# Performance work log

Measured on AMD Instinct MI355X. Metric: run time of the kernel, lower is better.

## Reference

```python
import jax, jax.numpy as jnp
import numpy as np

B, L, K = 4, 4096, 48
BIG = 1e9  # masked-out distance sentinel


def setup_inputs() -> dict:
    key = jax.random.key(0)
    k1, k2 = jax.random.split(key)
    # Backbone coords (B, L, 4, 3): N, CA, C, O. Scaled to Angstrom-ish magnitudes.
    X = jax.random.normal(k1, (B, L, 4, 3), dtype=jnp.float32) * 10.0
    mask = (jax.random.uniform(k2, (B, L)) > 0.1).astype(jnp.float32)
    return {"X": X, "mask": mask, "k_neighbors": K}


def reference(X, mask, k_neighbors):
    """GPU-friendly equivalent of precompute_knn_cpu:
    brute-force masked pairwise euclidean distances + top-k, with
    self-fill for invalid residues and the degenerate n_valid<=k batch case.
    Returns (D_neighbors (B,L,k) float, E_idx (B,L,k) int32).
    """
    Xca = X[:, :, 1, :]                       # (B, L, 3) CA atoms
    m = mask > 0                              # (B, L) bool valid
    # ||a-b||^2 = ||a||^2 + ||b||^2 - 2 a.b  (avoids (B,L,L,3) intermediate)
    x2 = jnp.sum(Xca * Xca, axis=-1)          # (B, L)
    D2 = x2[:, :, None] + x2[:, None, :] - 2.0 * jnp.einsum('bld,bmd->blm', Xca, Xca)
    D = jnp.sqrt(jnp.maximum(D2, 0.0))        # (B, L, L)
    # mask invalid key columns so they are never selected
    Dm = jnp.where(m[:, None, :], D, BIG)
    _, idx = jax.lax.top_k(-Dm, k_neighbors)  # k smallest distances, (B, L, k)
    self_idx = jnp.broadcast_to(jnp.arange(L, dtype=idx.dtype)[None, :, None],
                                (B, L, k_neighbors))
    n_valid = jnp.sum(m, axis=1)              # (B,)
    # degenerate batch: n_valid <= k -> every row filled with its own index
    degen = (n_valid <= k_neighbors)[:, None, None]
    # invalid rows -> self index; valid rows -> knn indices (already in original index space)
    E_idx = jnp.where(degen | (~m[:, :, None]), self_idx, idx)
    D_neighbors = jnp.take_along_axis(D, E_idx, axis=2)  # (B, L, k)
    return D_neighbors, E_idx
```

## Files before the change

### kernel.cpp

```cpp
#include <hip/hip_runtime.h>

typedef unsigned long long u64;

#define L_DIM 4096
#define B_DIM 4
#define KNN 48
#define CAP 512
#define INVALID_X2 1.0e30f
#define VALID_TH 1.0e29f
#define SLACK 8u
#define NT 256
#define NW 4
#define CPT 16
#define ROWS 2

__global__ __launch_bounds__(256) void prep_kernel(const float* __restrict__ X,
                                                   const float* __restrict__ mask,
                                                   float4* __restrict__ c4,
                                                   int* __restrict__ nvalid) {
#pragma clang fp contract(off)
    int i = blockIdx.x * 256 + threadIdx.x;
    const float4* X4 = (const float4*)X;
    float4 a = X4[3 * i];
    float4 bb = X4[3 * i + 1];
    float x = a.w, y = bb.x, z = bb.y;
    float x2 = __builtin_fmaf(z, z, __builtin_fmaf(y, y, x * x));
    float m = mask[i];
    c4[i] = make_float4(x, y, z, (m > 0.0f) ? x2 : INVALID_X2);
    unsigned long long bal = __ballot(m > 0.0f);
    if ((threadIdx.x & 63) == 0)
        atomicAdd(&nvalid[i >> 12], (int)__popcll(bal));
}

__device__ __forceinline__ unsigned wave_sort64(unsigned sv, int lane) {
#pragma unroll
    for (int k = 2; k <= 64; k <<= 1) {
#pragma unroll
        for (int j = k >> 1; j > 0; j >>= 1) {
            unsigned o = __shfl_xor(sv, j);
            unsigned mn = min(sv, o), mx = max(sv, o);
            bool asc = ((lane & k) == 0);
            bool low = ((lane & j) == 0);
            sv = (asc == low) ? mn : mx;
        }
    }
    return sv;
}

__global__ __launch_bounds__(NT) void knn_kernel(const float4* __restrict__ c4,
                                                 const int* __restrict__ nvalid,
                                                 float* __restrict__ dn,
                                                 float* __restrict__ ei) {
    __shared__ unsigned gmin[ROWS][64];
    __shared__ u64 surv[ROWS][CAP];
    __shared__ int cnt[ROWS];
    __shared__ unsigned Tsh[ROWS];

    const int row0 = blockIdx.x * ROWS;
    const int b = row0 >> 12;
    const int i0 = row0 & (L_DIM - 1);
    const int t = threadIdx.x;
    const int w = t >> 6, lane = t & 63;

    if (nvalid[b] <= KNN) {
        if (w < ROWS && lane < KNN) {
            dn[(size_t)(row0 + w) * KNN + lane] = 0.0f;
            ei[(size_t)(row0 + w) * KNN + lane] = (float)(i0 + w);
        }
        return;
    }

    const float4* cb = c4 + (size_t)b * L_DIM;
    const float4 q0 = cb[i0];
    const float4 q1 = cb[i0 + 1];
    const bool v0 = (q0.w < VALID_TH), v1 = (q1.w < VALID_TH);

    unsigned d20[CPT], d21[CPT];
    unsigned rmin0 = 0xFFFFFFFFu, rmin1 = 0xFFFFFFFFu;
    {
#pragma clang fp contract(off)
#pragma unroll
        for (int c = 0; c < CPT; ++c) {
            int j = c * NT + t;
            float4 pj = cb[j];
            float dota = __builtin_fmaf(pj.z, q0.z,
                         __builtin_fmaf(pj.y, q0.y, pj.x * q0.x));
            float dotb = __builtin_fmaf(pj.z, q1.z,
                         __builtin_fmaf(pj.y, q1.y, pj.x * q1.x));
            float d2a = fmaxf(__builtin_fmaf(-2.0f, dota, q0.w + pj.w), 0.0f);
            float d2b = fmaxf(__builtin_fmaf(-2.0f, dotb, q1.w + pj.w), 0.0f);
            d20[c] = __float_as_uint(d2a);
            d21[c] = __float_as_uint(d2b);
            rmin0 = min(rmin0, d20[c]);
            rmin1 = min(rmin1, d21[c]);
        }
    }

    {
        unsigned g0 = min(rmin0, __shfl_xor(rmin0, 1));
        g0 = min(g0, __shfl_xor(g0, 2));
        unsigned g1 = min(rmin1, __shfl_xor(rmin1, 1));
        g1 = min(g1, __shfl_xor(g1, 2));
        if ((lane & 3) == 0) {
            gmin[0][(w << 4) | (lane >> 2)] = g0;
            gmin[1][(w << 4) | (lane >> 2)] = g1;
        }
    }
    if (t < ROWS) cnt[t] = 0;
    __syncthreads();
    if (w < ROWS) {
        unsigned sv = wave_sort64(gmin[w][lane], lane);
        if (lane == KNN - 1) Tsh[w] = sv;
    }
    __syncthreads();
    const unsigned Tp0 = v0 ? (Tsh[0] + SLACK) : 0u;
    const unsigned Tp1 = v1 ? (Tsh[1] + SLACK) : 0u;

#pragma unroll
    for (int c = 0; c < CPT; ++c) {
        unsigned j = (unsigned)(c * NT + t);
        if (d20[c] <= Tp0) {
            int pos = atomicAdd(&cnt[0], 1);
            if (pos < CAP) {
                float d = sqrtf(__uint_as_float(d20[c]));
                surv[0][pos] = ((u64)__float_as_uint(d) << 32) | j;
            }
        }
        if (d21[c] <= Tp1) {
            int pos = atomicAdd(&cnt[1], 1);
            if (pos < CAP) {
                float d = sqrtf(__uint_as_float(d21[c]));
                surv[1][pos] = ((u64)__float_as_uint(d) << 32) | j;
            }
        }
    }
    __syncthreads();

#pragma unroll
    for (int r = 0; r < ROWS; ++r) {
        const bool vr = r ? v1 : v0;
        float* dnrow = dn + (size_t)(row0 + r) * KNN;
        float* eirow = ei + (size_t)(row0 + r) * KNN;
        if (!vr) {
            if (t < KNN) { dnrow[t] = 0.0f; eirow[t] = (float)(i0 + r); }
        } else {
            int S = cnt[r]; if (S > CAP) S = CAP;
            for (int c = t; c < S; c += NT) {
                u64 key = surv[r][c];
                int rank = 0;
                for (int s = 0; s < S; ++s) rank += (surv[r][s] < key);
                if (rank < KNN) {
                    dnrow[rank] = __uint_as_float((unsigned)(key >> 32));
                    eirow[rank] = (float)(key & 0xFFFFFFFFULL);
                }
            }
        }
    }
}

extern "C" void kernel_launch(void* const* d_in, const int* in_sizes, int n_in,
                              void* d_out, int out_size, void* d_ws, size_t ws_size,
                              hipStream_t stream) {
    const float* X = (const float*)d_in[0];
    const float* mask = (const float*)d_in[1];

    float* out = (float*)d_out;
    float* dn = out;
    float* ei = out + (size_t)B_DIM * L_DIM * KNN;

    char* ws = (char*)d_ws;
    float4* c4 = (float4*)ws;
    int* nv = (int*)(ws + (size_t)B_DIM * L_DIM * 16);

    hipMemsetAsync(nv, 0, B_DIM * sizeof(int), stream);
    prep_kernel<<<(B_DIM * L_DIM) / 256, 256, 0, stream>>>(X, mask, c4, nv);
    knn_kernel<<<(B_DIM * L_DIM) / ROWS, NT, 0, stream>>>(c4, nv, dn, ei);
}
```

Measured before the change: 72.09 us.

## Switch coordinates to SoA layout and compute distances with packed FP32 ops

The prep kernel now writes x, y, z and squared-norm/mask into four separate arrays instead of an interleaved float4 array. The distance kernel loads four consecutive points per thread with float4 loads from each array and computes two distances per instruction using v_pk_fma/v_pk_mul/v_pk_add, with v_min3 for the running minimum. The aim is to halve the VALU instruction count in the distance phase. The clamp to zero moves from every distance to only the threshold and candidate paths, and survivor indices are remapped for the new per-thread point ordering.

```diff
diff --git a/kernel.cpp b/kernel.cpp
--- a/kernel.cpp
+++ b/kernel.cpp
@@ -1,6 +1,7 @@
 #include <hip/hip_runtime.h>
 
 typedef unsigned long long u64;
+typedef float v2f __attribute__((ext_vector_type(2)));
 
 #define L_DIM 4096
 #define B_DIM 4
@@ -10,13 +11,28 @@
 #define VALID_TH 1.0e29f
 #define SLACK 8u
 #define NT 256
-#define NW 4
-#define CPT 16
+#define NIT 4
 #define ROWS 2
+
+__device__ __forceinline__ v2f pk_mul(v2f a, v2f b) {
+    v2f d; asm("v_pk_mul_f32 %0, %1, %2" : "=v"(d) : "v"(a), "v"(b)); return d;
+}
+__device__ __forceinline__ v2f pk_add(v2f a, v2f b) {
+    v2f d; asm("v_pk_add_f32 %0, %1, %2" : "=v"(d) : "v"(a), "v"(b)); return d;
+}
+__device__ __forceinline__ v2f pk_fma(v2f a, v2f b, v2f c) {
+    v2f d; asm("v_pk_fma_f32 %0, %1, %2, %3" : "=v"(d) : "v"(a), "v"(b), "v"(c)); return d;
+}
+__device__ __forceinline__ float min3f(float a, float b, float c) {
+    float d; asm("v_min3_f32 %0, %1, %2, %3" : "=v"(d) : "v"(a), "v"(b), "v"(c)); return d;
+}
 
 __global__ __launch_bounds__(256) void prep_kernel(const float* __restrict__ X,
                                                    const float* __restrict__ mask,
-                                                   float4* __restrict__ c4,
+                                                   float* __restrict__ xs,
+                                                   float* __restrict__ ys,
+                                                   float* __restrict__ zs,
+                                                   float* __restrict__ ws,
                                                    int* __restrict__ nvalid) {
 #pragma clang fp contract(off)
     int i = blockIdx.x * 256 + threadIdx.x;
@@ -26,7 +42,8 @@
     float x = a.w, y = bb.x, z = bb.y;
     float x2 = __builtin_fmaf(z, z, __builtin_fmaf(y, y, x * x));
     float m = mask[i];
-    c4[i] = make_float4(x, y, z, (m > 0.0f) ? x2 : INVALID_X2);
+    xs[i] = x; ys[i] = y; zs[i] = z;
+    ws[i] = (m > 0.0f) ? x2 : INVALID_X2;
     unsigned long long bal = __ballot(m > 0.0f);
     if ((threadIdx.x & 63) == 0)
         atomicAdd(&nvalid[i >> 12], (int)__popcll(bal));
@@ -47,7 +64,10 @@
     return sv;
 }
 
-__global__ __launch_bounds__(NT) void knn_kernel(const float4* __restrict__ c4,
+__global__ __launch_bounds__(NT) void knn_kernel(const float* __restrict__ xs,
+                                                 const float* __restrict__ ys,
+                                                 const float* __restrict__ zs,
+                                                 const float* __restrict__ ws,
                                                  const int* __restrict__ nvalid,
                                                  float* __restrict__ dn,
                                                  float* __restrict__ ei) {
@@ -70,40 +90,54 @@
         return;
     }
 
-    const float4* cb = c4 + (size_t)b * L_DIM;
-    const float4 q0 = cb[i0];
-    const float4 q1 = cb[i0 + 1];
-    const bool v0 = (q0.w < VALID_TH), v1 = (q1.w < VALID_TH);
-
-    unsigned d20[CPT], d21[CPT];
-    unsigned rmin0 = 0xFFFFFFFFu, rmin1 = 0xFFFFFFFFu;
+    const size_t bo = (size_t)b * L_DIM;
+    const float* xb = xs + bo; const float* yb = ys + bo;
+    const float* zb = zs + bo; const float* wb = ws + bo;
+
+    const float q0w = wb[i0], q1w = wb[i0 + 1];
+    const bool v0 = (q0w < VALID_TH), v1 = (q1w < VALID_TH);
+    const v2f qx0 = {xb[i0], xb[i0]},     qy0 = {yb[i0], yb[i0]},
+              qz0 = {zb[i0], zb[i0]},     qw0 = {q0w, q0w};
+    const v2f qx1 = {xb[i0+1], xb[i0+1]}, qy1 = {yb[i0+1], yb[i0+1]},
+              qz1 = {zb[i0+1], zb[i0+1]}, qw1 = {q1w, q1w};
+    const v2f m2 = {-2.0f, -2.0f};
+
+    v2f d2a[NIT * 2], d2b[NIT * 2];
+    float rmin0 = 3.402823466e38f, rmin1 = 3.402823466e38f;
+#pragma unroll
+    for (int c = 0; c < NIT; ++c) {
+        int off = c * (NT * 4) + t * 4;
+        float4 xv = *(const float4*)(xb + off);
+        float4 yv = *(const float4*)(yb + off);
+        float4 zv = *(const float4*)(zb + off);
+        float4 wv = *(const float4*)(wb + off);
+        v2f xlo = {xv.x, xv.y}, xhi = {xv.z, xv.w};
+        v2f ylo = {yv.x, yv.y}, yhi = {yv.z, yv.w};
+        v2f zlo = {zv.x, zv.y}, zhi = {zv.z, zv.w};
+        v2f wlo = {wv.x, wv.y}, whi = {wv.z, wv.w};
+
+        v2f dot0l = pk_fma(zlo, qz0, pk_fma(ylo, qy0, pk_mul(xlo, qx0)));
+        v2f dot0h = pk_fma(zhi, qz0, pk_fma(yhi, qy0, pk_mul(xhi, qx0)));
+        v2f dot1l = pk_fma(zlo, qz1, pk_fma(ylo, qy1, pk_mul(xlo, qx1)));
+        v2f dot1h = pk_fma(zhi, qz1, pk_fma(yhi, qy1, pk_mul(xhi, qx1)));
+        v2f d0l = pk_fma(m2, dot0l, pk_add(wlo, qw0));
+        v2f d0h = pk_fma(m2, dot0h, pk_add(whi, qw0));
+        v2f d1l = pk_fma(m2, dot1l, pk_add(wlo, qw1));
+        v2f d1h = pk_fma(m2, dot1h, pk_add(whi, qw1));
+        d2a[c * 2] = d0l; d2a[c * 2 + 1] = d0h;
+        d2b[c * 2] = d1l; d2b[c * 2 + 1] = d1h;
+        rmin0 = min3f(rmin0, d0l.x, d0l.y); rmin0 = min3f(rmin0, d0h.x, d0h.y);
+        rmin1 = min3f(rmin1, d1l.x, d1l.y); rmin1 = min3f(rmin1, d1h.x, d1h.y);
+    }
+
     {
-#pragma clang fp contract(off)
-#pragma unroll
-        for (int c = 0; c < CPT; ++c) {
-            int j = c * NT + t;
-            float4 pj = cb[j];
-            float dota = __builtin_fmaf(pj.z, q0.z,
-                         __builtin_fmaf(pj.y, q0.y, pj.x * q0.x));
-            float dotb = __builtin_fmaf(pj.z, q1.z,
-                         __builtin_fmaf(pj.y, q1.y, pj.x * q1.x));
-            float d2a = fmaxf(__builtin_fmaf(-2.0f, dota, q0.w + pj.w), 0.0f);
-            float d2b = fmaxf(__builtin_fmaf(-2.0f, dotb, q1.w + pj.w), 0.0f);
-            d20[c] = __float_as_uint(d2a);
-            d21[c] = __float_as_uint(d2b);
-            rmin0 = min(rmin0, d20[c]);
-            rmin1 = min(rmin1, d21[c]);
-        }
-    }
-
-    {
-        unsigned g0 = min(rmin0, __shfl_xor(rmin0, 1));
-        g0 = min(g0, __shfl_xor(g0, 2));
-        unsigned g1 = min(rmin1, __shfl_xor(rmin1, 1));
-        g1 = min(g1, __shfl_xor(g1, 2));
+        float g0 = fminf(rmin0, __shfl_xor(rmin0, 1));
+        g0 = fminf(g0, __shfl_xor(g0, 2));
+        float g1 = fminf(rmin1, __shfl_xor(rmin1, 1));
+        g1 = fminf(g1, __shfl_xor(g1, 2));
         if ((lane & 3) == 0) {
-            gmin[0][(w << 4) | (lane >> 2)] = g0;
-            gmin[1][(w << 4) | (lane >> 2)] = g1;
+            gmin[0][(w << 4) | (lane >> 2)] = __float_as_uint(fmaxf(g0, 0.0f));
+            gmin[1][(w << 4) | (lane >> 2)] = __float_as_uint(fmaxf(g1, 0.0f));
         }
     }
     if (t < ROWS) cnt[t] = 0;
@@ -113,24 +147,29 @@
         if (lane == KNN - 1) Tsh[w] = sv;
     }
     __syncthreads();
-    const unsigned Tp0 = v0 ? (Tsh[0] + SLACK) : 0u;
-    const unsigned Tp1 = v1 ? (Tsh[1] + SLACK) : 0u;
-
-#pragma unroll
-    for (int c = 0; c < CPT; ++c) {
-        unsigned j = (unsigned)(c * NT + t);
-        if (d20[c] <= Tp0) {
-            int pos = atomicAdd(&cnt[0], 1);
-            if (pos < CAP) {
-                float d = sqrtf(__uint_as_float(d20[c]));
-                surv[0][pos] = ((u64)__float_as_uint(d) << 32) | j;
+    const float Tf0 = v0 ? __uint_as_float(Tsh[0] + SLACK) : -3.0e38f;
+    const float Tf1 = v1 ? __uint_as_float(Tsh[1] + SLACK) : -3.0e38f;
+
+#pragma unroll
+    for (int c = 0; c < NIT * 2; ++c) {
+        unsigned jb = (unsigned)((c >> 1) * (NT * 4) + t * 4 + (c & 1) * 2);
+#pragma unroll
+        for (int h = 0; h < 2; ++h) {
+            float va = h ? d2a[c].y : d2a[c].x;
+            float vb = h ? d2b[c].y : d2b[c].x;
+            if (va <= Tf0) {
+                int pos = atomicAdd(&cnt[0], 1);
+                if (pos < CAP) {
+                    float d = sqrtf(fmaxf(va, 0.0f));
+                    surv[0][pos] = ((u64)__float_as_uint(d) << 32) | (jb + h);
+                }
             }
-        }
-        if (d21[c] <= Tp1) {
-            int pos = atomicAdd(&cnt[1], 1);
-            if (pos < CAP) {
-                float d = sqrtf(__uint_as_float(d21[c]));
-                surv[1][pos] = ((u64)__float_as_uint(d) << 32) | j;
+            if (vb <= Tf1) {
+                int pos = atomicAdd(&cnt[1], 1);
+                if (pos < CAP) {
+                    float d = sqrtf(fmaxf(vb, 0.0f));
+                    surv[1][pos] = ((u64)__float_as_uint(d) << 32) | (jb + h);
+                }
             }
         }
     }
@@ -168,11 +207,15 @@
     float* dn = out;
     float* ei = out + (size_t)B_DIM * L_DIM * KNN;
 
-    char* ws = (char*)d_ws;
-    float4* c4 = (float4*)ws;
-    int* nv = (int*)(ws + (size_t)B_DIM * L_DIM * 16);
+    const size_t BL = (size_t)B_DIM * L_DIM;
+    char* wsb = (char*)d_ws;
+    float* xs = (float*)wsb;
+    float* ys = (float*)(wsb + BL * 4);
+    float* zs = (float*)(wsb + BL * 8);
+    float* ws = (float*)(wsb + BL * 12);
+    int* nv = (int*)(wsb + BL * 16);
 
     hipMemsetAsync(nv, 0, B_DIM * sizeof(int), stream);
-    prep_kernel<<<(B_DIM * L_DIM) / 256, 256, 0, stream>>>(X, mask, c4, nv);
-    knn_kernel<<<(B_DIM * L_DIM) / ROWS, NT, 0, stream>>>(c4, nv, dn, ei);
-}
+    prep_kernel<<<(B_DIM * L_DIM) / 256, 256, 0, stream>>>(X, mask, xs, ys, zs, ws, nv);
+    knn_kernel<<<(B_DIM * L_DIM) / ROWS, NT, 0, stream>>>(xs, ys, zs, ws, nv, dn, ei);
+}
```

Result: slower. 79.44 us (+10.2%).

## Stash truncated 16-bit distance keys in LDS and recompute survivors

Applied to the files above, without the earlier changes.

Instead of keeping 32 squared distances per thread in registers, the kernel packs the upper 16 bits of both rows' distance bit patterns into one LDS word per candidate. In the filter pass it compares these truncated keys against the truncated threshold and only reloads coordinates and recomputes exact distances for candidates that pass. The survivor capacity is cut from 512 to 384. The aim is lower register pressure and higher occupancy, at the cost of extra LDS traffic, more false-positive survivors from the coarser 16-bit filter, recomputation work, and a higher chance of overflowing the smaller survivor buffer.

```diff
diff --git a/kernel.cpp b/kernel.cpp
--- a/kernel.cpp
+++ b/kernel.cpp
@@ -5,7 +5,7 @@
 #define L_DIM 4096
 #define B_DIM 4
 #define KNN 48
-#define CAP 512
+#define CAP 384
 #define INVALID_X2 1.0e30f
 #define VALID_TH 1.0e29f
 #define SLACK 8u
@@ -51,6 +51,7 @@
                                                  const int* __restrict__ nvalid,
                                                  float* __restrict__ dn,
                                                  float* __restrict__ ei) {
+    __shared__ unsigned stash[CPT][NT];
     __shared__ unsigned gmin[ROWS][64];
     __shared__ u64 surv[ROWS][CAP];
     __shared__ int cnt[ROWS];
@@ -75,7 +76,6 @@
     const float4 q1 = cb[i0 + 1];
     const bool v0 = (q0.w < VALID_TH), v1 = (q1.w < VALID_TH);
 
-    unsigned d20[CPT], d21[CPT];
     unsigned rmin0 = 0xFFFFFFFFu, rmin1 = 0xFFFFFFFFu;
     {
 #pragma clang fp contract(off)
@@ -89,10 +89,11 @@
                          __builtin_fmaf(pj.y, q1.y, pj.x * q1.x));
             float d2a = fmaxf(__builtin_fmaf(-2.0f, dota, q0.w + pj.w), 0.0f);
             float d2b = fmaxf(__builtin_fmaf(-2.0f, dotb, q1.w + pj.w), 0.0f);
-            d20[c] = __float_as_uint(d2a);
-            d21[c] = __float_as_uint(d2b);
-            rmin0 = min(rmin0, d20[c]);
-            rmin1 = min(rmin1, d21[c]);
+            unsigned ba = __float_as_uint(d2a);
+            unsigned bbts = __float_as_uint(d2b);
+            stash[c][t] = (bbts & 0xFFFF0000u) | (ba >> 16);
+            rmin0 = min(rmin0, ba);
+            rmin1 = min(rmin1, bbts);
         }
     }
 
@@ -115,22 +116,40 @@
     __syncthreads();
     const unsigned Tp0 = v0 ? (Tsh[0] + SLACK) : 0u;
     const unsigned Tp1 = v1 ? (Tsh[1] + SLACK) : 0u;
+    const unsigned T16a = Tp0 >> 16, T16b = Tp1 >> 16;
 
+    {
+#pragma clang fp contract(off)
 #pragma unroll
-    for (int c = 0; c < CPT; ++c) {
-        unsigned j = (unsigned)(c * NT + t);
-        if (d20[c] <= Tp0) {
-            int pos = atomicAdd(&cnt[0], 1);
-            if (pos < CAP) {
-                float d = sqrtf(__uint_as_float(d20[c]));
-                surv[0][pos] = ((u64)__float_as_uint(d) << 32) | j;
-            }
-        }
-        if (d21[c] <= Tp1) {
-            int pos = atomicAdd(&cnt[1], 1);
-            if (pos < CAP) {
-                float d = sqrtf(__uint_as_float(d21[c]));
-                surv[1][pos] = ((u64)__float_as_uint(d) << 32) | j;
+        for (int c = 0; c < CPT; ++c) {
+            unsigned v = stash[c][t];
+            unsigned ha = v & 0xFFFFu;
+            unsigned hb = v >> 16;
+            bool pa = (ha <= T16a) && v0;
+            bool pb = (hb <= T16b) && v1;
+            if (pa || pb) {
+                int j = c * NT + t;
+                float4 pj = cb[j];
+                if (pa) {
+                    float dota = __builtin_fmaf(pj.z, q0.z,
+                                 __builtin_fmaf(pj.y, q0.y, pj.x * q0.x));
+                    float d2a = fmaxf(__builtin_fmaf(-2.0f, dota, q0.w + pj.w), 0.0f);
+                    int pos = atomicAdd(&cnt[0], 1);
+                    if (pos < CAP) {
+                        float d = sqrtf(d2a);
+                        surv[0][pos] = ((u64)__float_as_uint(d) << 32) | (unsigned)j;
+                    }
+                }
+                if (pb) {
+                    float dotb = __builtin_fmaf(pj.z, q1.z,
+                                 __builtin_fmaf(pj.y, q1.y, pj.x * q1.x));
+                    float d2b = fmaxf(__builtin_fmaf(-2.0f, dotb, q1.w + pj.w), 0.0f);
+                    int pos = atomicAdd(&cnt[1], 1);
+                    if (pos < CAP) {
+                        float d = sqrtf(d2b);
+                        surv[1][pos] = ((u64)__float_as_uint(d) << 32) | (unsigned)j;
+                    }
+                }
             }
         }
     }
@@ -172,7 +191,7 @@
     float4* c4 = (float4*)ws;
     int* nv = (int*)(ws + (size_t)B_DIM * L_DIM * 16);
 
-    hipMemsetAsync(nv, 0, B_DIM * sizeof(int), stream);
+    (void)hipMemsetAsync(nv, 0, B_DIM * sizeof(int), stream);
     prep_kernel<<<(B_DIM * L_DIM) / 256, 256, 0, stream>>>(X, mask, c4, nv);
     knn_kernel<<<(B_DIM * L_DIM) / ROWS, NT, 0, stream>>>(c4, nv, dn, ei);
 }
```

Result: slower. 88.52 us (+22.8%).
